# Performance work log

Hardware: AMD Instinct MI355X
Metric: run time of the kernel (lower is better)

The kernel has to match this reference:

```python
import jax, jax.numpy as jnp
import numpy as np

EPS = 1e-5

def _bn(x, w, b, rm, rv):
    # eval-mode BatchNorm over channel axis (x: [..., C] broadcastable)
    return (x - rm) * (w * jax.lax.rsqrt(rv + EPS)) + b

def setup_inputs() -> dict:
    key = jax.random.key(0)
    ks = jax.random.split(key, 20)
    B, C, H, W = 2, 64, 96, 96
    Cq = C // 8  # query/key channels
    Cr = C // 8  # SE reduction channels
    s = 0.05
    inp = {
        'x': jax.random.normal(ks[0], (B, C, H, W), jnp.float32),
        'wq': jax.random.normal(ks[1], (Cq, C), jnp.float32) * s,
        'bq': jnp.zeros((Cq,), jnp.float32),
        'wk': jax.random.normal(ks[2], (Cq, C), jnp.float32) * s,
        'bk': jnp.zeros((Cq,), jnp.float32),
        'wv': jax.random.normal(ks[3], (C, C), jnp.float32) * s,
        'bv': jnp.zeros((C,), jnp.float32),
        'gamma': jnp.full((1,), 0.5, jnp.float32),
        'bn_w': jnp.ones((C,), jnp.float32),
        'bn_b': jnp.zeros((C,), jnp.float32),
        'bn_rm': jax.random.normal(ks[4], (C,), jnp.float32) * 0.1,
        'bn_rv': jax.random.uniform(ks[5], (C,), jnp.float32) + 0.5,
        'se_w1': jax.random.normal(ks[6], (Cr, C), jnp.float32) * s,
        'se_b1': jnp.zeros((Cr,), jnp.float32),
        'se_bn1_w': jnp.ones((Cr,), jnp.float32),
        'se_bn1_b': jnp.zeros((Cr,), jnp.float32),
        'se_bn1_rm': jax.random.normal(ks[7], (Cr,), jnp.float32) * 0.1,
        'se_bn1_rv': jax.random.uniform(ks[8], (Cr,), jnp.float32) + 0.5,
        'se_w2': jax.random.normal(ks[9], (C, Cr), jnp.float32) * s,
        'se_b2': jnp.zeros((C,), jnp.float32),
        'se_bn2_w': jnp.ones((C,), jnp.float32),
        'se_bn2_b': jnp.zeros((C,), jnp.float32),
        'se_bn2_rm': jax.random.normal(ks[10], (C,), jnp.float32) * 0.1,
        'se_bn2_rv': jax.random.uniform(ks[11], (C,), jnp.float32) + 0.5,
    }
    return inp

def reference(x, wq, bq, wk, bk, wv, bv, gamma, bn_w, bn_b, bn_rm, bn_rv,
              se_w1, se_b1, se_bn1_w, se_bn1_b, se_bn1_rm, se_bn1_rv,
              se_w2, se_b2, se_bn2_w, se_bn2_b, se_bn2_rm, se_bn2_rv):
    B, C, H, W = x.shape
    N = H * W
    xf = x.reshape(B, C, N)
    # PAM branch: 1x1 conv projections
    q = jnp.einsum('oc,bcn->bno', wq, xf) + bq            # [B,N,C/8]
    k = jnp.einsum('oc,bcn->bon', wk, xf) + bk[:, None]    # [B,C/8,N]
    v = jnp.einsum('oc,bcn->bon', wv, xf) + bv[:, None]    # [B,C,N]
    energy = jnp.einsum('bno,bom->bnm', q, k)              # [B,N,N]
    attn = jax.nn.softmax(energy, axis=-1)
    # out[b,c,i] = sum_j v[b,c,j] * attn[b,i,j]  (bmm(V, attn^T))
    out = jnp.einsum('bcj,bij->bci', v, attn)
    out = gamma[0] * out
    out = _bn(out, bn_w[:, None], bn_b[:, None], bn_rm[:, None], bn_rv[:, None])
    pam = out.reshape(B, C, H, W)
    # SE branch: GAP + 1x1 conv-bn-relu x2, multiplicative gate
    a = xf.mean(axis=2)                                    # [B,C]
    a1 = jax.nn.relu(_bn(a @ se_w1.T + se_b1, se_bn1_w, se_bn1_b, se_bn1_rm, se_bn1_rv))
    a2 = jax.nn.relu(_bn(a1 @ se_w2.T + se_b2, se_bn2_w, se_bn2_b, se_bn2_rm, se_bn2_rv))
    se = x * a2[:, :, None, None]
    return x + se + pam
```

## Files before the change

kernel.cpp:

```cpp
#include <hip/hip_runtime.h>
#include <hip/hip_bf16.h>

#define B_SZ   2
#define C_CH   64
#define NQ     8
#define NPIX   9216
#define NJC    288
#define QBLKS  288
#define KPART  8
#define KEYS_P 1152
#define NCHUNK 18
#define SM_F   2080
#define NP4    2304

typedef short bf16x8 __attribute__((ext_vector_type(8)));
typedef float f32x4  __attribute__((ext_vector_type(4)));
typedef unsigned u32x4 __attribute__((ext_vector_type(4)));
typedef unsigned uint2v __attribute__((ext_vector_type(2)));

static __device__ __forceinline__ unsigned pack2bf(float a, float b){
    union { __hip_bfloat16 h; unsigned short us; } ca, cb;
    ca.h = __float2bfloat16(a); cb.h = __float2bfloat16(b);
    return (unsigned)ca.us | ((unsigned)cb.us << 16);
}

static __device__ __forceinline__ unsigned short bf16b(float a){
    union { __hip_bfloat16 h; unsigned short us; } c;
    c.h = __float2bfloat16(a); return c.us;
}

__global__ __launch_bounds__(256) void prep_kernel(
    const float* __restrict__ x,
    const float* __restrict__ wq, const float* __restrict__ bq,
    const float* __restrict__ wk, const float* __restrict__ bk,
    const float* __restrict__ wv, const float* __restrict__ bv,
    __hip_bfloat16* __restrict__ qp, __hip_bfloat16* __restrict__ kp,
    __hip_bfloat16* __restrict__ vswz, float* __restrict__ amean)
{
    const int blk = blockIdx.x, tid = threadIdx.x;
    if (blk < 144){
        int t  = blk*256 + tid;
        int n  = (t % NP4) * 4;
        int c8 = (t / NP4) & 7;
        int b  = t / (NP4*8);
        c8 = __builtin_amdgcn_readfirstlane(c8);
        b  = __builtin_amdgcn_readfirstlane(b);
        float acc[8][4];
#pragma unroll
        for (int k = 0; k < 8; ++k){
            float bvv = bv[c8*8 + k];
            acc[k][0] = bvv; acc[k][1] = bvv; acc[k][2] = bvv; acc[k][3] = bvv;
        }
#pragma unroll 4
        for (int ci = 0; ci < C_CH; ++ci){
            const float4 xv = *reinterpret_cast<const float4*>(
                x + (size_t)(b*C_CH + ci)*NPIX + n);
#pragma unroll
            for (int k = 0; k < 8; ++k){
                float w = wv[(c8*8 + k)*C_CH + ci];
                acc[k][0] = fmaf(xv.x, w, acc[k][0]);
                acc[k][1] = fmaf(xv.y, w, acc[k][1]);
                acc[k][2] = fmaf(xv.z, w, acc[k][2]);
                acc[k][3] = fmaf(xv.w, w, acc[k][3]);
            }
        }
#pragma unroll
        for (int k = 0; k < 8; ++k){
            int c = c8*8 + k;
            size_t base = ((size_t)((b*NJC + (n >> 5))*4 + (c >> 4)))*512
                        + ((c & 15)*32) + (n & 31);
            unsigned long long wpk =
                (unsigned long long)pack2bf(acc[k][0], acc[k][1]) |
                ((unsigned long long)pack2bf(acc[k][2], acc[k][3]) << 32);
            *reinterpret_cast<unsigned long long*>(vswz + base) = wpk;
        }
    } else if (blk < 180){
        int t  = (blk - 144)*256 + tid;
        int n  = (t % NP4) * 4;
        int o8 = (t / NP4) & 1;
        int b  = t / (NP4*2);
        o8 = __builtin_amdgcn_readfirstlane(o8);
        b  = __builtin_amdgcn_readfirstlane(b);
        const bool isq = (o8 == 0);
        const float* w    = isq ? wq : wk;
        const float* bias = isq ? bq : bk;
        float acc[8][4];
#pragma unroll
        for (int k = 0; k < 8; ++k){
            float bb = bias[k];
            acc[k][0] = bb; acc[k][1] = bb; acc[k][2] = bb; acc[k][3] = bb;
        }
#pragma unroll 4
        for (int ci = 0; ci < C_CH; ++ci){
            const float4 xv = *reinterpret_cast<const float4*>(
                x + (size_t)(b*C_CH + ci)*NPIX + n);
#pragma unroll
            for (int k = 0; k < 8; ++k){
                float wv_ = w[k*C_CH + ci];
                acc[k][0] = fmaf(xv.x, wv_, acc[k][0]);
                acc[k][1] = fmaf(xv.y, wv_, acc[k][1]);
                acc[k][2] = fmaf(xv.z, wv_, acc[k][2]);
                acc[k][3] = fmaf(xv.w, wv_, acc[k][3]);
            }
        }
        if (isq){
#pragma unroll
            for (int k = 0; k < 8; ++k)
#pragma unroll
                for (int px = 0; px < 4; ++px) acc[k][px] *= 1.44269504f;
        }
        __hip_bfloat16* dst = isq ? qp : kp;
#pragma unroll
        for (int px = 0; px < 4; ++px){
            bf16x8 row;
#pragma unroll
            for (int k = 0; k < 8; ++k) row[k] = (short)bf16b(acc[k][px]);
            *reinterpret_cast<bf16x8*>(dst + ((size_t)(b*NPIX + n + px))*NQ) = row;
        }
    } else {
        int bc = blk - 180;
        float s = 0.f;
        for (int i = tid; i < NPIX; i += 256) s += x[(size_t)bc*NPIX + i];
#pragma unroll
        for (int o = 32; o > 0; o >>= 1) s += __shfl_down(s, o, 64);
        __shared__ float red[4];
        if ((tid & 63) == 0) red[tid >> 6] = s;
        __syncthreads();
        if (tid == 0) amean[bc] = (red[0] + red[1] + red[2] + red[3]) * (1.f / (float)NPIX);
    }
}

__global__ __launch_bounds__(512, 4) void flash_fused(
    const __hip_bfloat16* __restrict__ qp,
    const __hip_bfloat16* __restrict__ kp,
    const __hip_bfloat16* __restrict__ vswz,
    const float* __restrict__ amean,
    const float* __restrict__ sw1, const float* __restrict__ sb1,
    const float* __restrict__ s1w, const float* __restrict__ s1b,
    const float* __restrict__ s1m, const float* __restrict__ s1v,
    const float* __restrict__ sw2, const float* __restrict__ sb2,
    const float* __restrict__ s2w, const float* __restrict__ s2b,
    const float* __restrict__ s2m, const float* __restrict__ s2v,
    const float* __restrict__ x,
    const float* __restrict__ gamma,
    const float* __restrict__ bnw, const float* __restrict__ bnb,
    const float* __restrict__ bnm, const float* __restrict__ bnv,
    float* __restrict__ out)
{
    __shared__ __align__(16) float sm[4*SM_F];

    const int qt2 = blockIdx.x, b = blockIdx.y;
    const int p  = threadIdx.x >> 6;
    const int l  = threadIdx.x & 63;
    const int lq = l & 15;
    const int lg = l >> 4;
    const int vlane = lq*32 + lg*8;

    float a1r;
    {
        int r8 = l & 7;
        float s = sb1[r8];
#pragma unroll 8
        for (int c = 0; c < C_CH; ++c)
            s = fmaf(amean[b*C_CH + c], sw1[r8*C_CH + c], s);
        s = (s - s1m[r8]) * (s1w[r8] * rsqrtf(s1v[r8] + 1e-5f)) + s1b[r8];
        a1r = fmaxf(s, 0.f);
    }

    bf16x8 zf = {0,0,0,0,0,0,0,0};
    bf16x8 qfrag[2];
#pragma unroll
    for (int qi = 0; qi < 2; ++qi){
        qfrag[qi] = zf;
        if (lg == 0)
            qfrag[qi] = *reinterpret_cast<const bf16x8*>(
                qp + (size_t)(b*NPIX + qt2*32 + qi*16 + lq) * NQ);
    }

    bf16x8 ones;
#pragma unroll
    for (int i = 0; i < 8; ++i) ones[i] = (short)0x3F80;

    f32x4 Of[2][4];
#pragma unroll
    for (int qi = 0; qi < 2; ++qi)
#pragma unroll
        for (int i = 0; i < 4; ++i) Of[qi][i] = (f32x4){0.f, 0.f, 0.f, 0.f};
    f32x4 Lf[2];
    Lf[0] = (f32x4){0.f, 0.f, 0.f, 0.f};
    Lf[1] = (f32x4){0.f, 0.f, 0.f, 0.f};

    for (int ch = 0; ch < NCHUNK; ++ch){
        const int j0  = p*KEYS_P + ch*64;
        const int jcb = b*NJC + (j0 >> 5);

        bf16x8 kf[4];
#pragma unroll
        for (int jt = 0; jt < 4; ++jt){
            kf[jt] = zf;
            if (lg == 0)
                kf[jt] = *reinterpret_cast<const bf16x8*>(kp + (size_t)(b*NPIX + j0 + jt*16 + lq) * NQ);
        }
        bf16x8 vf[2][4];
#pragma unroll
        for (int kc = 0; kc < 2; ++kc)
#pragma unroll
            for (int ct = 0; ct < 4; ++ct)
                vf[kc][ct] = *reinterpret_cast<const bf16x8*>(
                    vswz + ((size_t)((jcb + kc)*4 + ct))*512 + vlane);

#pragma unroll
        for (int qi = 0; qi < 2; ++qi){
            f32x4 Sf[4];
#pragma unroll
            for (int jt = 0; jt < 4; ++jt)
                Sf[jt] = __builtin_amdgcn_mfma_f32_16x16x32_bf16(kf[jt], qfrag[qi], (f32x4){0.f,0.f,0.f,0.f}, 0, 0, 0);

            unsigned D[4][2];
#pragma unroll
            for (int jt = 0; jt < 4; ++jt){
                D[jt][0] = pack2bf(exp2f(Sf[jt][0]), exp2f(Sf[jt][1]));
                D[jt][1] = pack2bf(exp2f(Sf[jt][2]), exp2f(Sf[jt][3]));
            }

#pragma unroll
            for (int kc = 0; kc < 2; ++kc){
                unsigned o0, o1, o2, o3;
                {
                    uint2v r1 = __builtin_amdgcn_permlane32_swap(D[2*kc][0], D[2*kc+1][0], false, false);
                    uint2v r2 = __builtin_amdgcn_permlane16_swap(r1[0], r1[1], false, false);
                    o0 = r2[0]; o2 = r2[1];
                }
                {
                    uint2v r1 = __builtin_amdgcn_permlane32_swap(D[2*kc][1], D[2*kc+1][1], false, false);
                    uint2v r2 = __builtin_amdgcn_permlane16_swap(r1[0], r1[1], false, false);
                    o1 = r2[0]; o3 = r2[1];
                }
                u32x4 pu; pu[0] = o0; pu[1] = o1; pu[2] = o2; pu[3] = o3;
                bf16x8 pf = __builtin_bit_cast(bf16x8, pu);
#pragma unroll
                for (int ct = 0; ct < 4; ++ct)
                    Of[qi][ct] = __builtin_amdgcn_mfma_f32_16x16x32_bf16(vf[kc][ct], pf, Of[qi][ct], 0, 0, 0);
                Lf[qi] = __builtin_amdgcn_mfma_f32_16x16x32_bf16(ones, pf, Lf[qi], 0, 0, 0);
            }
        }
    }

    if (p >= 4){
        const int ps = p - 4;
#pragma unroll
        for (int qi = 0; qi < 2; ++qi)
#pragma unroll
            for (int ct = 0; ct < 4; ++ct)
#pragma unroll
                for (int r = 0; r < 4; ++r)
                    sm[ps*SM_F + qi*1024 + (ct*4 + r)*64 + l] = Of[qi][ct][r];
        if (l < 16){
            sm[ps*SM_F + 2048 + lq]      = Lf[0][0];
            sm[ps*SM_F + 2048 + 16 + lq] = Lf[1][0];
        }
    }
    __syncthreads();
    if (p < 4){
#pragma unroll
        for (int qi = 0; qi < 2; ++qi)
#pragma unroll
            for (int ct = 0; ct < 4; ++ct)
#pragma unroll
                for (int r = 0; r < 4; ++r)
                    sm[p*SM_F + qi*1024 + (ct*4 + r)*64 + l] += Of[qi][ct][r];
        if (l < 16){
            sm[p*SM_F + 2048 + lq]      += Lf[0][0];
            sm[p*SM_F + 2048 + 16 + lq] += Lf[1][0];
        }
    }
    __syncthreads();

    {
        const int w8 = threadIdx.x >> 6;
        const int qi = w8 >> 2;
        const int ct = w8 & 3;
        float gam = gamma[0];

        float a1g[8];
#pragma unroll
        for (int j = 0; j < 8; ++j) a1g[j] = __shfl(a1r, (l & 56) | j, 64);
        float a2v[4];
#pragma unroll
        for (int r = 0; r < 4; ++r){
            int c = ct*16 + lg*4 + r;
            float s = sb2[c];
#pragma unroll
            for (int j = 0; j < 8; ++j) s = fmaf(a1g[j], sw2[c*NQ + j], s);
            s = (s - s2m[c]) * (s2w[c] * rsqrtf(s2v[c] + 1e-5f)) + s2b[c];
            a2v[r] = fmaxf(s, 0.f);
        }

        float L = 0.f;
#pragma unroll
        for (int q = 0; q < 4; ++q) L += sm[q*SM_F + 2048 + qi*16 + lq];
        float invL = 1.f / L;
        int n = qt2*32 + qi*16 + lq;
#pragma unroll
        for (int r = 0; r < 4; ++r){
            float O = 0.f;
#pragma unroll
            for (int q = 0; q < 4; ++q) O += sm[q*SM_F + qi*1024 + (ct*4 + r)*64 + l];
            int c = ct*16 + lg*4 + r;
            float pam = gam * O * invL;
            pam = (pam - bnm[c]) * (bnw[c] * rsqrtf(bnv[c] + 1e-5f)) + bnb[c];
            float xv = x[(size_t)(b*C_CH + c)*NPIX + n];
            out[(size_t)(b*C_CH + c)*NPIX + n] = fmaf(xv, a2v[r], xv + pam);
        }
    }
}

extern "C" void kernel_launch(void* const* d_in, const int* in_sizes, int n_in,
                              void* d_out, int out_size, void* d_ws, size_t ws_size,
                              hipStream_t stream)
{
    const float* x     = (const float*)d_in[0];
    const float* wq    = (const float*)d_in[1];
    const float* bq    = (const float*)d_in[2];
    const float* wk    = (const float*)d_in[3];
    const float* bk    = (const float*)d_in[4];
    const float* wv    = (const float*)d_in[5];
    const float* bv    = (const float*)d_in[6];
    const float* gamma = (const float*)d_in[7];
    const float* bnw   = (const float*)d_in[8];
    const float* bnb   = (const float*)d_in[9];
    const float* bnm   = (const float*)d_in[10];
    const float* bnv   = (const float*)d_in[11];
    const float* sw1   = (const float*)d_in[12];
    const float* sb1   = (const float*)d_in[13];
    const float* s1w   = (const float*)d_in[14];
    const float* s1b   = (const float*)d_in[15];
    const float* s1m   = (const float*)d_in[16];
    const float* s1v   = (const float*)d_in[17];
    const float* sw2   = (const float*)d_in[18];
    const float* sb2   = (const float*)d_in[19];
    const float* s2w   = (const float*)d_in[20];
    const float* s2b   = (const float*)d_in[21];
    const float* s2m   = (const float*)d_in[22];
    const float* s2v   = (const float*)d_in[23];

    size_t off = 0;
    auto give = [&](size_t bytes) -> void* {
        void* r = (char*)d_ws + off;
        off += (bytes + 255) & ~(size_t)255;
        return r;
    };
    __hip_bfloat16* qp   = (__hip_bfloat16*)give((size_t)B_SZ*NPIX*NQ*2);
    __hip_bfloat16* kp   = (__hip_bfloat16*)give((size_t)B_SZ*NPIX*NQ*2);
    __hip_bfloat16* vswz = (__hip_bfloat16*)give((size_t)B_SZ*C_CH*NPIX*2);
    float* amean = (float*)give((size_t)B_SZ*C_CH*4);

    prep_kernel<<<dim3(308), dim3(256), 0, stream>>>(x, wq, bq, wk, bk, wv, bv,
                                                     qp, kp, vswz, amean);
    flash_fused<<<dim3(QBLKS, B_SZ), dim3(512), 0, stream>>>(
        qp, kp, vswz, amean,
        sw1, sb1, s1w, s1b, s1m, s1v,
        sw2, sb2, s2w, s2b, s2m, s2v,
        x, gamma, bnw, bnb, bnm, bnv, (float*)d_out);
}
```

Baseline: 211.7 us.

## Double-buffer K/V register loads, relax launch bounds, use packed bf16 convert

```diff
diff --git a/kernel.cpp b/kernel.cpp
--- a/kernel.cpp
+++ b/kernel.cpp
@@ -12,6 +12,8 @@
 #define NCHUNK 18
 #define SM_F   2080
 #define NP4    2304
+#define KSTEP  (64*NQ)
+#define VSTEP  4096
 
 typedef short bf16x8 __attribute__((ext_vector_type(8)));
 typedef float f32x4  __attribute__((ext_vector_type(4)));
@@ -19,14 +21,9 @@
 typedef unsigned uint2v __attribute__((ext_vector_type(2)));
 
 static __device__ __forceinline__ unsigned pack2bf(float a, float b){
-    union { __hip_bfloat16 h; unsigned short us; } ca, cb;
-    ca.h = __float2bfloat16(a); cb.h = __float2bfloat16(b);
-    return (unsigned)ca.us | ((unsigned)cb.us << 16);
-}
-
-static __device__ __forceinline__ unsigned short bf16b(float a){
-    union { __hip_bfloat16 h; unsigned short us; } c;
-    c.h = __float2bfloat16(a); return c.us;
+    unsigned r;
+    asm("v_cvt_pk_bf16_f32 %0, %1, %2" : "=v"(r) : "v"(a), "v"(b));
+    return r;
 }
 
 __global__ __launch_bounds__(256) void prep_kernel(
@@ -112,10 +109,12 @@
         __hip_bfloat16* dst = isq ? qp : kp;
 #pragma unroll
         for (int px = 0; px < 4; ++px){
-            bf16x8 row;
-#pragma unroll
-            for (int k = 0; k < 8; ++k) row[k] = (short)bf16b(acc[k][px]);
-            *reinterpret_cast<bf16x8*>(dst + ((size_t)(b*NPIX + n + px))*NQ) = row;
+            u32x4 row;
+            row[0] = pack2bf(acc[0][px], acc[1][px]);
+            row[1] = pack2bf(acc[2][px], acc[3][px]);
+            row[2] = pack2bf(acc[4][px], acc[5][px]);
+            row[3] = pack2bf(acc[6][px], acc[7][px]);
+            *reinterpret_cast<u32x4*>(dst + ((size_t)(b*NPIX + n + px))*NQ) = row;
         }
     } else {
         int bc = blk - 180;
@@ -130,7 +129,7 @@
     }
 }
 
-__global__ __launch_bounds__(512, 4) void flash_fused(
+__global__ __launch_bounds__(512, 2) void flash_fused(
     const __hip_bfloat16* __restrict__ qp,
     const __hip_bfloat16* __restrict__ kp,
     const __hip_bfloat16* __restrict__ vswz,
@@ -156,17 +155,6 @@
     const int lg = l >> 4;
     const int vlane = lq*32 + lg*8;
 
-    float a1r;
-    {
-        int r8 = l & 7;
-        float s = sb1[r8];
-#pragma unroll 8
-        for (int c = 0; c < C_CH; ++c)
-            s = fmaf(amean[b*C_CH + c], sw1[r8*C_CH + c], s);
-        s = (s - s1m[r8]) * (s1w[r8] * rsqrtf(s1v[r8] + 1e-5f)) + s1b[r8];
-        a1r = fmaxf(s, 0.f);
-    }
-
     bf16x8 zf = {0,0,0,0,0,0,0,0};
     bf16x8 qfrag[2];
 #pragma unroll
@@ -190,39 +178,40 @@
     Lf[0] = (f32x4){0.f, 0.f, 0.f, 0.f};
     Lf[1] = (f32x4){0.f, 0.f, 0.f, 0.f};
 
-    for (int ch = 0; ch < NCHUNK; ++ch){
-        const int j0  = p*KEYS_P + ch*64;
-        const int jcb = b*NJC + (j0 >> 5);
-
-        bf16x8 kf[4];
+    const __hip_bfloat16* kptr = kp + ((size_t)(b*NPIX + p*KEYS_P + lq))*NQ;
+    const __hip_bfloat16* vptr = vswz + ((size_t)(b*NJC + p*(KEYS_P/32)))*4*512 + vlane;
+
+    bf16x8 kfa[4], vfa[2][4];
+    bf16x8 kfb[4], vfb[2][4];
+
+    auto loadK = [&](bf16x8 (&dst)[4], const __hip_bfloat16* ptr){
 #pragma unroll
         for (int jt = 0; jt < 4; ++jt){
-            kf[jt] = zf;
+            dst[jt] = zf;
             if (lg == 0)
-                kf[jt] = *reinterpret_cast<const bf16x8*>(kp + (size_t)(b*NPIX + j0 + jt*16 + lq) * NQ);
-        }
-        bf16x8 vf[2][4];
+                dst[jt] = *reinterpret_cast<const bf16x8*>(ptr + jt*16*NQ);
+        }
+    };
+    auto loadV = [&](bf16x8 (&dst)[2][4], const __hip_bfloat16* ptr){
 #pragma unroll
         for (int kc = 0; kc < 2; ++kc)
 #pragma unroll
             for (int ct = 0; ct < 4; ++ct)
-                vf[kc][ct] = *reinterpret_cast<const bf16x8*>(
-                    vswz + ((size_t)((jcb + kc)*4 + ct))*512 + vlane);
-
+                dst[kc][ct] = *reinterpret_cast<const bf16x8*>(ptr + (kc*4 + ct)*512);
+    };
+    auto compute = [&](bf16x8 (&kfc)[4], bf16x8 (&vfc)[2][4]){
 #pragma unroll
         for (int qi = 0; qi < 2; ++qi){
             f32x4 Sf[4];
 #pragma unroll
             for (int jt = 0; jt < 4; ++jt)
-                Sf[jt] = __builtin_amdgcn_mfma_f32_16x16x32_bf16(kf[jt], qfrag[qi], (f32x4){0.f,0.f,0.f,0.f}, 0, 0, 0);
-
+                Sf[jt] = __builtin_amdgcn_mfma_f32_16x16x32_bf16(kfc[jt], qfrag[qi], (f32x4){0.f,0.f,0.f,0.f}, 0, 0, 0);
             unsigned D[4][2];
 #pragma unroll
             for (int jt = 0; jt < 4; ++jt){
                 D[jt][0] = pack2bf(exp2f(Sf[jt][0]), exp2f(Sf[jt][1]));
                 D[jt][1] = pack2bf(exp2f(Sf[jt][2]), exp2f(Sf[jt][3]));
             }
-
 #pragma unroll
             for (int kc = 0; kc < 2; ++kc){
                 unsigned o0, o1, o2, o3;
@@ -240,10 +229,36 @@
                 bf16x8 pf = __builtin_bit_cast(bf16x8, pu);
 #pragma unroll
                 for (int ct = 0; ct < 4; ++ct)
-                    Of[qi][ct] = __builtin_amdgcn_mfma_f32_16x16x32_bf16(vf[kc][ct], pf, Of[qi][ct], 0, 0, 0);
+                    Of[qi][ct] = __builtin_amdgcn_mfma_f32_16x16x32_bf16(vfc[kc][ct], pf, Of[qi][ct], 0, 0, 0);
                 Lf[qi] = __builtin_amdgcn_mfma_f32_16x16x32_bf16(ones, pf, Lf[qi], 0, 0, 0);
             }
         }
+    };
+
+    loadK(kfa, kptr); loadV(vfa, vptr);
+    kptr += KSTEP; vptr += VSTEP;
+
+    for (int it = 0; it < (NCHUNK - 2)/2; ++it){
+        loadK(kfb, kptr); loadV(vfb, vptr);
+        kptr += KSTEP; vptr += VSTEP;
+        compute(kfa, vfa);
+        loadK(kfa, kptr); loadV(vfa, vptr);
+        kptr += KSTEP; vptr += VSTEP;
+        compute(kfb, vfb);
+    }
+    loadK(kfb, kptr); loadV(vfb, vptr);
+    compute(kfa, vfa);
+    compute(kfb, vfb);
+
+    float a1r;
+    {
+        int r8 = l & 7;
+        float s = sb1[r8];
+#pragma unroll 8
+        for (int c = 0; c < C_CH; ++c)
+            s = fmaf(amean[b*C_CH + c], sw1[r8*C_CH + c], s);
+        s = (s - s1m[r8]) * (s1w[r8] * rsqrtf(s1v[r8] + 1e-5f)) + s1b[r8];
+        a1r = fmaxf(s, 0.f);
     }
 
     if (p >= 4){
```

Measured after the change: 204.6 us. 3.3% less time.
